# Kernel optimization log

Hardware: AMD Instinct MI355X
Metric: run time of the kernel (lower is better)

The kernel has to match this reference:

```python
import jax, jax.numpy as jnp
import numpy as np

EPS = 1e-5  # torch nn.LayerNorm default

def _ln(x, g, b):
    # LayerNorm over last dim with per-position affine params g, b (broadcastable)
    m = jnp.mean(x, axis=-1, keepdims=True)
    v = jnp.mean((x - m) ** 2, axis=-1, keepdims=True)
    return (x - m) * jax.lax.rsqrt(v + EPS) * g + b

def _mlp_ln(s, W1, b1, W2, b2, g, b):
    # Linear -> SiLU -> Linear -> LayerNorm
    h = jax.nn.silu(s @ W1 + b1) @ W2 + b2
    return _ln(h, g, b)

def setup_inputs() -> dict:
    key = jax.random.key(0)
    B, S, D = 4, 2048, 1024
    MEM, NOI, RES = 512, 64, 32
    ks = jax.random.split(key, 40)
    ki = iter(range(40))
    def nrm(shape, scale=0.02):
        return (jax.random.normal(ks[next(ki)], shape, jnp.float32) * scale)
    def gamma(shape):
        return jnp.ones(shape, jnp.float32) + nrm(shape)
    inp = {
        'x': jax.random.normal(ks[next(ki)], (B, S, D), jnp.float32),
        'pathway_ids': jax.random.randint(ks[next(ki)], (B, S), 0, 1000),
        'compartment_ids': jax.random.randint(ks[next(ki)], (B, S), 0, 5),
        'time_steps': jax.random.randint(ks[next(ki)], (B, S), 0, 5),
        'scale_type': jax.random.randint(ks[next(ki)], (B, S), 0, 3),
        'memory_state': jax.random.normal(ks[next(ki)], (B, MEM), jnp.float32),
        'noise_state': jax.random.normal(ks[next(ki)], (B, NOI), jnp.float32),
        'resource_state': jax.random.normal(ks[next(ki)], (B, RES), jnp.float32),
        # per-pathway / compartment / time / scale LayerNorm affine tables
        'pw_g': gamma((1000, D)), 'pw_b': nrm((1000, D)),
        'cp_g': gamma((5, D)), 'cp_b': nrm((5, D)),
        'tm_g': gamma((5, D)), 'tm_b': nrm((5, D)),
        'ms_g': gamma((3, D)), 'ms_b': nrm((3, D)),
        # memory / stochastic / resource MLP+LN stacks
        'mem_W1': nrm((MEM, D)), 'mem_b1': jnp.zeros((D,)), 'mem_W2': nrm((D, D)), 'mem_b2': jnp.zeros((D,)), 'mem_g': gamma((D,)), 'mem_be': jnp.zeros((D,)),
        'noi_W1': nrm((NOI, D)), 'noi_b1': jnp.zeros((D,)), 'noi_W2': nrm((D, D)), 'noi_b2': jnp.zeros((D,)), 'noi_g': gamma((D,)), 'noi_be': jnp.zeros((D,)),
        'res_W1': nrm((RES, D)), 'res_b1': jnp.zeros((D,)), 'res_W2': nrm((D, D)), 'res_b2': jnp.zeros((D,)), 'res_g': gamma((D,)), 'res_be': jnp.zeros((D,)),
        # integration MLP+LN
        'int_W1': nrm((6 * D, D)), 'int_b1': jnp.zeros((D,)), 'int_W2': nrm((D, D)), 'int_b2': jnp.zeros((D,)), 'int_g': gamma((D,)), 'int_be': jnp.zeros((D,)),
        'aw': jnp.ones((6,), jnp.float32) / 6.0,
    }
    return inp

def reference(x, pathway_ids, compartment_ids, time_steps, scale_type,
              memory_state, noise_state, resource_state,
              pw_g, pw_b, cp_g, cp_b, tm_g, tm_b, ms_g, ms_b,
              mem_W1, mem_b1, mem_W2, mem_b2, mem_g, mem_be,
              noi_W1, noi_b1, noi_W2, noi_b2, noi_g, noi_be,
              res_W1, res_b1, res_W2, res_b2, res_g, res_be,
              int_W1, int_b1, int_W2, int_b2, int_g, int_be, aw):
    # hierarchical: pathway-indexed LN, then compartment-indexed LN on its output
    h = _ln(x, pw_g[pathway_ids], pw_b[pathway_ids])
    h = _ln(h, cp_g[compartment_ids], cp_b[compartment_ids])
    # temporal: time-step-indexed LN of x
    t = _ln(x, tm_g[time_steps], tm_b[time_steps])
    # state-conditioned additive effects, broadcast over seq
    m = x + _mlp_ln(memory_state, mem_W1, mem_b1, mem_W2, mem_b2, mem_g, mem_be)[:, None, :]
    n = x + _mlp_ln(noise_state, noi_W1, noi_b1, noi_W2, noi_b2, noi_g, noi_be)[:, None, :]
    r = x + _mlp_ln(resource_state, res_W1, res_b1, res_W2, res_b2, res_g, res_be)[:, None, :]
    # multiscale: scale-indexed LN (scale in {0,1,2})
    s = _ln(x, ms_g[scale_type], ms_b[scale_type])
    w = jax.nn.softmax(aw)
    cat = jnp.concatenate([w[0] * h, w[1] * t, w[2] * m, w[3] * n, w[4] * r, w[5] * s], axis=-1)
    return _mlp_ln(cat, int_W1, int_b1, int_W2, int_b2, int_g, int_be)
```

## Files before the change

### kernel.cpp

```cpp
#include <hip/hip_runtime.h>
#include <cstdint>
#include <cstddef>

#define EPS_LN 1e-5f

typedef short bf16x8 __attribute__((ext_vector_type(8)));
typedef float f32x4 __attribute__((ext_vector_type(4)));
typedef unsigned int u32_gl __attribute__((address_space(1)));
typedef unsigned int u32_ld __attribute__((address_space(3)));

__device__ __forceinline__ unsigned short f2bf(float f) {
  union { float f; unsigned u; } v; v.f = f;
  unsigned r = v.u + 0x7fffu + ((v.u >> 16) & 1u);
  return (unsigned short)(r >> 16);
}

__device__ __forceinline__ float block_sum256(float v, float* red) {
  for (int m = 32; m > 0; m >>= 1) v += __shfl_xor(v, m, 64);
  const int lane = threadIdx.x & 63, w = threadIdx.x >> 6;
  if (lane == 0) red[w] = v;
  __syncthreads();
  float r = red[0] + red[1] + red[2] + red[3];
  __syncthreads();
  return r;
}

__global__ void prep_w(const float* __restrict__ aw, float* __restrict__ w) {
  if (threadIdx.x == 0) {
    float m = aw[0];
    for (int i = 1; i < 6; ++i) m = fmaxf(m, aw[i]);
    float e[6], s = 0.f;
    for (int i = 0; i < 6; ++i) { e[i] = __expf(aw[i] - m); s += e[i]; }
    for (int i = 0; i < 6; ++i) w[i] = e[i] / s;
  }
}

__global__ __launch_bounds__(256) void init_h1(
    const float* __restrict__ mb1, const float* __restrict__ nb1,
    const float* __restrict__ rb1, float* __restrict__ H1pre) {
  const int idx = blockIdx.x * 256 + threadIdx.x;
  const int row = idx >> 10, j = idx & 1023;
  const int st = row >> 2;
  const float* b1 = st == 0 ? mb1 : st == 1 ? nb1 : rb1;
  H1pre[idx] = b1[j];
}

__global__ __launch_bounds__(256) void state_h1_acc(
    const float* __restrict__ mem, const float* __restrict__ noi, const float* __restrict__ res,
    const float* __restrict__ mW1, const float* __restrict__ nW1, const float* __restrict__ rW1,
    float* __restrict__ H1pre) {
  const int chunk = blockIdx.x, ks = blockIdx.y;
  const int j = chunk * 128 + (threadIdx.x & 127);
  const int half = threadIdx.x >> 7;
  int st, k0, klen, sstride;
  const float* W1; const float* sp;
  if (ks < 8)       { st = 0; W1 = mW1; sp = mem; sstride = 512; k0 = ks * 64 + half * 32; klen = 32; }
  else if (ks == 8) { st = 1; W1 = nW1; sp = noi; sstride = 64;  k0 = half * 32;           klen = 32; }
  else              { st = 2; W1 = rW1; sp = res; sstride = 32;  k0 = half * 16;           klen = 16; }
  float a0 = 0.f, a1 = 0.f, a2 = 0.f, a3 = 0.f;
  const float* wp = W1 + (size_t)k0 * 1024 + j;
  for (int it = 0; it < klen; ++it) {
    const float wv = wp[(size_t)it * 1024];
    const int k = k0 + it;
    a0 += sp[k] * wv;
    a1 += sp[sstride + k] * wv;
    a2 += sp[2 * sstride + k] * wv;
    a3 += sp[3 * sstride + k] * wv;
  }
  __shared__ float part[4][128];
  const int jl = threadIdx.x & 127;
  if (half) { part[0][jl] = a0; part[1][jl] = a1; part[2][jl] = a2; part[3][jl] = a3; }
  __syncthreads();
  if (!half) {
    atomicAdd(&H1pre[(size_t)(st * 4 + 0) * 1024 + j], a0 + part[0][jl]);
    atomicAdd(&H1pre[(size_t)(st * 4 + 1) * 1024 + j], a1 + part[1][jl]);
    atomicAdd(&H1pre[(size_t)(st * 4 + 2) * 1024 + j], a2 + part[2][jl]);
    atomicAdd(&H1pre[(size_t)(st * 4 + 3) * 1024 + j], a3 + part[3][jl]);
  }
}

__global__ __launch_bounds__(256) void h1_silu(
    const float* __restrict__ H1pre, float* __restrict__ H1) {
  const int idx = blockIdx.x * 256 + threadIdx.x;
  const float h = H1pre[idx];
  H1[idx] = h / (1.f + __expf(-h));
}

__global__ __launch_bounds__(256) void init_ys(
    const float* __restrict__ mb2, const float* __restrict__ nb2,
    const float* __restrict__ rb2, float* __restrict__ Ys) {
  const int idx = blockIdx.x * 256 + threadIdx.x;
  const int row = idx >> 10, j = idx & 1023;
  const int st = row >> 2;
  const float* b2 = st == 0 ? mb2 : st == 1 ? nb2 : rb2;
  Ys[idx] = b2[j];
}

__global__ __launch_bounds__(256) void state_y_acc(
    const float* __restrict__ H1,
    const float* __restrict__ mW2, const float* __restrict__ nW2, const float* __restrict__ rW2,
    float* __restrict__ Ys) {
  const int chunk = blockIdx.x, ks = blockIdx.y, st = blockIdx.z;
  const float* W2 = st == 0 ? mW2 : st == 1 ? nW2 : rW2;
  const int j = chunk * 128 + (threadIdx.x & 127);
  const int half = threadIdx.x >> 7;
  const int k0 = ks * 64 + half * 32;
  const float* h1 = H1 + (size_t)st * 4096;
  float a0 = 0.f, a1 = 0.f, a2 = 0.f, a3 = 0.f;
  const float* wp = W2 + (size_t)k0 * 1024 + j;
  for (int it = 0; it < 32; ++it) {
    const float wv = wp[(size_t)it * 1024];
    const int k = k0 + it;
    a0 += h1[k] * wv;
    a1 += h1[1024 + k] * wv;
    a2 += h1[2048 + k] * wv;
    a3 += h1[3072 + k] * wv;
  }
  __shared__ float part[4][128];
  const int jl = threadIdx.x & 127;
  if (half) { part[0][jl] = a0; part[1][jl] = a1; part[2][jl] = a2; part[3][jl] = a3; }
  __syncthreads();
  if (!half) {
    atomicAdd(&Ys[(size_t)(st * 4 + 0) * 1024 + j], a0 + part[0][jl]);
    atomicAdd(&Ys[(size_t)(st * 4 + 1) * 1024 + j], a1 + part[1][jl]);
    atomicAdd(&Ys[(size_t)(st * 4 + 2) * 1024 + j], a2 + part[2][jl]);
    atomicAdd(&Ys[(size_t)(st * 4 + 3) * 1024 + j], a3 + part[3][jl]);
  }
}

__global__ __launch_bounds__(256) void state_ln(
    const float* __restrict__ Ys,
    const float* __restrict__ mg, const float* __restrict__ mbe,
    const float* __restrict__ ng, const float* __restrict__ nbe,
    const float* __restrict__ rg, const float* __restrict__ rbe,
    const float* __restrict__ w, float* __restrict__ mnrv) {
  __shared__ float red[4];
  const int st = blockIdx.x >> 2, b = blockIdx.x & 3;
  const float* g  = st == 0 ? mg  : st == 1 ? ng  : rg;
  const float* be = st == 0 ? mbe : st == 1 ? nbe : rbe;
  const float* y = Ys + (size_t)blockIdx.x * 1024;
  const int j = threadIdx.x * 4;
  float4 yv4 = *(const float4*)(y + j);
  float yv[4] = { yv4.x, yv4.y, yv4.z, yv4.w };
  float s = yv[0] + yv[1] + yv[2] + yv[3];
  float ss = yv[0]*yv[0] + yv[1]*yv[1] + yv[2]*yv[2] + yv[3]*yv[3];
  s = block_sum256(s, red);
  ss = block_sum256(ss, red);
  const float mu = s * (1.f / 1024.f);
  const float rstd = rsqrtf(ss * (1.f / 1024.f) - mu * mu + EPS_LN);
  float4 g4 = *(const float4*)(g + j);
  float4 b4 = *(const float4*)(be + j);
  const float sc = w[2 + st];
  float* out = mnrv + (size_t)b * 3072 + st * 1024;
  out[j]     = ((yv[0] - mu) * rstd * g4.x + b4.x) * sc;
  out[j + 1] = ((yv[1] - mu) * rstd * g4.y + b4.y) * sc;
  out[j + 2] = ((yv[2] - mu) * rstd * g4.z + b4.z) * sc;
  out[j + 3] = ((yv[3] - mu) * rstd * g4.w + b4.w) * sc;
}

__global__ __launch_bounds__(256) void init_bias1(
    const float* __restrict__ ib1, float* __restrict__ bias1) {
  const int j = blockIdx.x * 256 + threadIdx.x;
  bias1[j] = ib1[j & 1023];
}

__global__ __launch_bounds__(256) void bias1_kernel(
    const float* __restrict__ mnrv, const float* __restrict__ iW1,
    float* __restrict__ bias1) {
  const int chunk = blockIdx.x, ks = blockIdx.y;
  const int j = chunk * 128 + (threadIdx.x & 127);
  const int half = threadIdx.x >> 7;
  const int g0 = ks * 64 + half * 32;
  float acc0 = 0.f, acc1 = 0.f, acc2 = 0.f, acc3 = 0.f;
  const float* wp = iW1 + (size_t)(2048 + g0) * 1024 + j;
  for (int it = 0; it < 32; ++it) {
    const int g = g0 + it;
    const float wv = wp[(size_t)it * 1024];
    acc0 += mnrv[g] * wv;
    acc1 += mnrv[3072 + g] * wv;
    acc2 += mnrv[6144 + g] * wv;
    acc3 += mnrv[9216 + g] * wv;
  }
  __shared__ float part[4][128];
  const int jl = threadIdx.x & 127;
  if (half) { part[0][jl] = acc0; part[1][jl] = acc1; part[2][jl] = acc2; part[3][jl] = acc3; }
  __syncthreads();
  if (!half) {
    atomicAdd(&bias1[j],        acc0 + part[0][jl]);
    atomicAdd(&bias1[1024 + j], acc1 + part[1][jl]);
    atomicAdd(&bias1[2048 + j], acc2 + part[2][jl]);
    atomicAdd(&bias1[3072 + j], acc3 + part[3][jl]);
  }
}

__global__ __launch_bounds__(256) void build_w1t(
    const float* __restrict__ W1, const float* __restrict__ w,
    unsigned short* __restrict__ W1T) {
  __shared__ float tile[32][33];
  const int k0 = blockIdx.x * 32, n0 = blockIdx.y * 32;
  const int r = threadIdx.x >> 3;
  const int c = (threadIdx.x & 7) * 4;
  const int kk = k0 + r;
  float v[4];
  if (kk < 2048) {
    const float s = (kk < 1024) ? w[0] : w[1];
    float4 a = *(const float4*)(W1 + (size_t)kk * 1024 + n0 + c);
    v[0] = s * a.x; v[1] = s * a.y; v[2] = s * a.z; v[3] = s * a.w;
  } else if (kk < 3072) {
    const float s2 = w[2], s3 = w[3], s4 = w[4];
    float4 a = *(const float4*)(W1 + (size_t)kk * 1024 + n0 + c);
    float4 bq = *(const float4*)(W1 + (size_t)(kk + 1024) * 1024 + n0 + c);
    float4 cq = *(const float4*)(W1 + (size_t)(kk + 2048) * 1024 + n0 + c);
    v[0] = s2 * a.x + s3 * bq.x + s4 * cq.x;
    v[1] = s2 * a.y + s3 * bq.y + s4 * cq.y;
    v[2] = s2 * a.z + s3 * bq.z + s4 * cq.z;
    v[3] = s2 * a.w + s3 * bq.w + s4 * cq.w;
  } else {
    const float s = w[5];
    float4 a = *(const float4*)(W1 + (size_t)(kk + 2048) * 1024 + n0 + c);
    v[0] = s * a.x; v[1] = s * a.y; v[2] = s * a.z; v[3] = s * a.w;
  }
  tile[r][c] = v[0]; tile[r][c + 1] = v[1]; tile[r][c + 2] = v[2]; tile[r][c + 3] = v[3];
  __syncthreads();
  const int nl = threadIdx.x >> 3;
  const int k4 = (threadIdx.x & 7) * 4;
  ushort4 o;
  o.x = f2bf(tile[k4][nl]);     o.y = f2bf(tile[k4 + 1][nl]);
  o.z = f2bf(tile[k4 + 2][nl]); o.w = f2bf(tile[k4 + 3][nl]);
  *(ushort4*)(W1T + (size_t)(n0 + nl) * 4096 + k0 + k4) = o;
}

__global__ __launch_bounds__(256) void build_w2t(
    const float* __restrict__ W2, unsigned short* __restrict__ W2T) {
  __shared__ float tile[32][33];
  const int k0 = blockIdx.x * 32, n0 = blockIdx.y * 32;
  const int r = threadIdx.x >> 3, c = (threadIdx.x & 7) * 4;
  float4 a = *(const float4*)(W2 + (size_t)(k0 + r) * 1024 + n0 + c);
  tile[r][c] = a.x; tile[r][c + 1] = a.y; tile[r][c + 2] = a.z; tile[r][c + 3] = a.w;
  __syncthreads();
  const int nl = threadIdx.x >> 3, k4 = (threadIdx.x & 7) * 4;
  ushort4 o;
  o.x = f2bf(tile[k4][nl]);     o.y = f2bf(tile[k4 + 1][nl]);
  o.z = f2bf(tile[k4 + 2][nl]); o.w = f2bf(tile[k4 + 3][nl]);
  *(ushort4*)(W2T + (size_t)(n0 + nl) * 1024 + k0 + k4) = o;
}

__global__ __launch_bounds__(256) void build_cat(
    const float* __restrict__ x,
    const int* __restrict__ pid_, const int* __restrict__ cid_,
    const int* __restrict__ tid_, const int* __restrict__ sid_,
    const float* __restrict__ pwg, const float* __restrict__ pwb,
    const float* __restrict__ cpg, const float* __restrict__ cpb,
    const float* __restrict__ tmg, const float* __restrict__ tmb,
    const float* __restrict__ msg, const float* __restrict__ msb,
    unsigned short* __restrict__ cat4) {
  __shared__ float red[4];
  const int row = blockIdx.x;
  const int j = threadIdx.x * 4;
  float4 xv4 = *(const float4*)(x + (size_t)row * 1024 + j);
  float xv[4] = { xv4.x, xv4.y, xv4.z, xv4.w };
  float s = xv[0] + xv[1] + xv[2] + xv[3];
  float ss = xv[0]*xv[0] + xv[1]*xv[1] + xv[2]*xv[2] + xv[3]*xv[3];
  s = block_sum256(s, red);
  ss = block_sum256(ss, red);
  const float mu = s * (1.f / 1024.f);
  const float rstd = rsqrtf(ss * (1.f / 1024.f) - mu * mu + EPS_LN);
  float xh[4];
  for (int q = 0; q < 4; ++q) xh[q] = (xv[q] - mu) * rstd;
  const int pid = pid_[row], cid = cid_[row], tmi = tid_[row], msi = sid_[row];
  unsigned short* crow = cat4 + (size_t)row * 4096;

  float4 g4 = *(const float4*)(pwg + (size_t)pid * 1024 + j);
  float4 b4 = *(const float4*)(pwb + (size_t)pid * 1024 + j);
  float h1[4];
  h1[0] = xh[0] * g4.x + b4.x; h1[1] = xh[1] * g4.y + b4.y;
  h1[2] = xh[2] * g4.z + b4.z; h1[3] = xh[3] * g4.w + b4.w;
  float s1 = h1[0] + h1[1] + h1[2] + h1[3];
  float ss1 = h1[0]*h1[0] + h1[1]*h1[1] + h1[2]*h1[2] + h1[3]*h1[3];
  s1 = block_sum256(s1, red);
  ss1 = block_sum256(ss1, red);
  const float mu1 = s1 * (1.f / 1024.f);
  const float rstd1 = rsqrtf(ss1 * (1.f / 1024.f) - mu1 * mu1 + EPS_LN);
  g4 = *(const float4*)(cpg + (size_t)cid * 1024 + j);
  b4 = *(const float4*)(cpb + (size_t)cid * 1024 + j);
  ushort4 o;
  o.x = f2bf((h1[0] - mu1) * rstd1 * g4.x + b4.x);
  o.y = f2bf((h1[1] - mu1) * rstd1 * g4.y + b4.y);
  o.z = f2bf((h1[2] - mu1) * rstd1 * g4.z + b4.z);
  o.w = f2bf((h1[3] - mu1) * rstd1 * g4.w + b4.w);
  *(ushort4*)(crow + j) = o;

  g4 = *(const float4*)(tmg + (size_t)tmi * 1024 + j);
  b4 = *(const float4*)(tmb + (size_t)tmi * 1024 + j);
  o.x = f2bf(xh[0] * g4.x + b4.x); o.y = f2bf(xh[1] * g4.y + b4.y);
  o.z = f2bf(xh[2] * g4.z + b4.z); o.w = f2bf(xh[3] * g4.w + b4.w);
  *(ushort4*)(crow + 1024 + j) = o;

  o.x = f2bf(xv[0]); o.y = f2bf(xv[1]); o.z = f2bf(xv[2]); o.w = f2bf(xv[3]);
  *(ushort4*)(crow + 2048 + j) = o;

  g4 = *(const float4*)(msg + (size_t)msi * 1024 + j);
  b4 = *(const float4*)(msb + (size_t)msi * 1024 + j);
  o.x = f2bf(xh[0] * g4.x + b4.x); o.y = f2bf(xh[1] * g4.y + b4.y);
  o.z = f2bf(xh[2] * g4.z + b4.z); o.w = f2bf(xh[3] * g4.w + b4.w);
  *(ushort4*)(crow + 3072 + j) = o;
}

template <int EPI>
__global__ __launch_bounds__(256, 2) void gemm_bt(
    const unsigned short* __restrict__ A, const unsigned short* __restrict__ BT,
    const float* __restrict__ bias, void* __restrict__ out, int K) {
  __shared__ unsigned short At[128 * 32];
  __shared__ unsigned short Bt[128 * 32];
  const int t = threadIdx.x;
  const int lane = t & 63;
  const int wave = t >> 6;
  const int wr = wave >> 1, wc = wave & 1;
  const int quad = lane >> 4, l16 = lane & 15;
  const int bm = blockIdx.x, bn = blockIdx.y;
  const unsigned short* Ab = A + (size_t)bm * 128 * K;
  const unsigned short* Bb = BT + (size_t)bn * 128 * K;
  const int r0 = t >> 2, c0 = (t & 3) * 8;
  f32x4 acc[4][4];
#pragma unroll
  for (int i = 0; i < 4; ++i)
#pragma unroll
    for (int jj = 0; jj < 4; ++jj) { f32x4 z = {0.f, 0.f, 0.f, 0.f}; acc[i][jj] = z; }

  for (int kt = 0; kt < K; kt += 32) {
    __builtin_amdgcn_global_load_lds(
        (const u32_gl*)(Ab + (size_t)r0 * K + kt + c0),
        (u32_ld*)(At + t * 8), 16, 0, 0);
    __builtin_amdgcn_global_load_lds(
        (const u32_gl*)(Ab + (size_t)(r0 + 64) * K + kt + c0),
        (u32_ld*)(At + (256 + t) * 8), 16, 0, 0);
    __builtin_amdgcn_global_load_lds(
        (const u32_gl*)(Bb + (size_t)r0 * K + kt + c0),
        (u32_ld*)(Bt + t * 8), 16, 0, 0);
    __builtin_amdgcn_global_load_lds(
        (const u32_gl*)(Bb + (size_t)(r0 + 64) * K + kt + c0),
        (u32_ld*)(Bt + (256 + t) * 8), 16, 0, 0);
    __syncthreads();
    bf16x8 aF[4], bF[4];
#pragma unroll
    for (int mi = 0; mi < 4; ++mi)
      aF[mi] = *(const bf16x8*)(At + (wr * 64 + mi * 16 + l16) * 32 + quad * 8);
#pragma unroll
    for (int ni = 0; ni < 4; ++ni)
      bF[ni] = *(const bf16x8*)(Bt + (wc * 64 + ni * 16 + l16) * 32 + quad * 8);
#pragma unroll
    for (int mi = 0; mi < 4; ++mi)
#pragma unroll
      for (int ni = 0; ni < 4; ++ni)
        acc[mi][ni] = __builtin_amdgcn_mfma_f32_16x16x32_bf16(aF[mi], bF[ni], acc[mi][ni], 0, 0, 0);
    __syncthreads();
  }
#pragma unroll
  for (int mi = 0; mi < 4; ++mi) {
#pragma unroll
    for (int ni = 0; ni < 4; ++ni) {
      const int col = bn * 128 + wc * 64 + ni * 16 + l16;
#pragma unroll
      for (int r = 0; r < 4; ++r) {
        const int row = bm * 128 + wr * 64 + mi * 16 + quad * 4 + r;
        float v = acc[mi][ni][r];
        if (EPI == 1) {
          v += bias[(size_t)(row >> 11) * 1024 + col];
          v = v / (1.f + __expf(-v));
          ((unsigned short*)out)[(size_t)row * 1024 + col] = f2bf(v);
        } else {
          v += bias[col];
          ((float*)out)[(size_t)row * 1024 + col] = v;
        }
      }
    }
  }
}

__global__ __launch_bounds__(256) void final_ln(
    const float* __restrict__ Y, const float* __restrict__ g,
    const float* __restrict__ be, float* __restrict__ out) {
  __shared__ float red[4];
  const int row = blockIdx.x;
  const int j = threadIdx.x * 4;
  float4 yv4 = *(const float4*)(Y + (size_t)row * 1024 + j);
  float yv[4] = { yv4.x, yv4.y, yv4.z, yv4.w };
  float s = yv[0] + yv[1] + yv[2] + yv[3];
  float ss = yv[0]*yv[0] + yv[1]*yv[1] + yv[2]*yv[2] + yv[3]*yv[3];
  s = block_sum256(s, red);
  ss = block_sum256(ss, red);
  const float mu = s * (1.f / 1024.f);
  const float rstd = rsqrtf(ss * (1.f / 1024.f) - mu * mu + EPS_LN);
  float4 g4 = *(const float4*)(g + j);
  float4 b4 = *(const float4*)(be + j);
  float4 o;
  o.x = (yv[0] - mu) * rstd * g4.x + b4.x;
  o.y = (yv[1] - mu) * rstd * g4.y + b4.y;
  o.z = (yv[2] - mu) * rstd * g4.z + b4.z;
  o.w = (yv[3] - mu) * rstd * g4.w + b4.w;
  *(float4*)(out + (size_t)row * 1024 + j) = o;
}

extern "C" void kernel_launch(void* const* d_in, const int* in_sizes, int n_in,
                              void* d_out, int out_size, void* d_ws, size_t ws_size,
                              hipStream_t stream) {
  const float* x   = (const float*)d_in[0];
  const int*   pid = (const int*)d_in[1];
  const int*   cid = (const int*)d_in[2];
  const int*   tms = (const int*)d_in[3];
  const int*   sct = (const int*)d_in[4];
  const float* mem = (const float*)d_in[5];
  const float* noi = (const float*)d_in[6];
  const float* res = (const float*)d_in[7];
  const float* pwg = (const float*)d_in[8];
  const float* pwb = (const float*)d_in[9];
  const float* cpg = (const float*)d_in[10];
  const float* cpb = (const float*)d_in[11];
  const float* tmg = (const float*)d_in[12];
  const float* tmb = (const float*)d_in[13];
  const float* msg = (const float*)d_in[14];
  const float* msb = (const float*)d_in[15];
  const float* mW1 = (const float*)d_in[16]; const float* mb1 = (const float*)d_in[17];
  const float* mW2 = (const float*)d_in[18]; const float* mb2 = (const float*)d_in[19];
  const float* mg  = (const float*)d_in[20]; const float* mbe = (const float*)d_in[21];
  const float* nW1 = (const float*)d_in[22]; const float* nb1 = (const float*)d_in[23];
  const float* nW2 = (const float*)d_in[24]; const float* nb2 = (const float*)d_in[25];
  const float* ng  = (const float*)d_in[26]; const float* nbe = (const float*)d_in[27];
  const float* rW1 = (const float*)d_in[28]; const float* rb1 = (const float*)d_in[29];
  const float* rW2 = (const float*)d_in[30]; const float* rb2 = (const float*)d_in[31];
  const float* rg  = (const float*)d_in[32]; const float* rbe = (const float*)d_in[33];
  const float* iW1 = (const float*)d_in[34]; const float* ib1 = (const float*)d_in[35];
  const float* iW2 = (const float*)d_in[36]; const float* ib2 = (const float*)d_in[37];
  const float* ig  = (const float*)d_in[38]; const float* ibe = (const float*)d_in[39];
  const float* aw  = (const float*)d_in[40];

  char* ws = (char*)d_ws;
  float* w6    = (float*)ws;
  float* H1pre = w6 + 16;
  float* H1    = H1pre + 12288;
  float* Ys    = H1 + 12288;
  float* mnrv  = Ys + 12288;
  float* bias1 = mnrv + 12288;
  unsigned short* W1T  = (unsigned short*)(ws + (1ull << 20));
  unsigned short* W2T  = (unsigned short*)(ws + (9ull << 20));
  unsigned short* cat4 = (unsigned short*)(ws + (11ull << 20));
  unsigned short* Hb   = (unsigned short*)(ws + (75ull << 20));
  float* Ybuf          = (float*)cat4;

  prep_w<<<1, 64, 0, stream>>>(aw, w6);
  init_h1<<<48, 256, 0, stream>>>(mb1, nb1, rb1, H1pre);
  state_h1_acc<<<dim3(8, 10), 256, 0, stream>>>(mem, noi, res, mW1, nW1, rW1, H1pre);
  h1_silu<<<48, 256, 0, stream>>>(H1pre, H1);
  init_ys<<<48, 256, 0, stream>>>(mb2, nb2, rb2, Ys);
  state_y_acc<<<dim3(8, 16, 3), 256, 0, stream>>>(H1, mW2, nW2, rW2, Ys);
  state_ln<<<12, 256, 0, stream>>>(Ys, mg, mbe, ng, nbe, rg, rbe, w6, mnrv);
  init_bias1<<<16, 256, 0, stream>>>(ib1, bias1);
  bias1_kernel<<<dim3(8, 48), 256, 0, stream>>>(mnrv, iW1, bias1);
  build_w1t<<<dim3(128, 32), 256, 0, stream>>>(iW1, w6, W1T);
  build_w2t<<<dim3(32, 32), 256, 0, stream>>>(iW2, W2T);
  build_cat<<<8192, 256, 0, stream>>>(x, pid, cid, tms, sct,
                                      pwg, pwb, cpg, cpb, tmg, tmb, msg, msb, cat4);
  gemm_bt<1><<<dim3(64, 8), 256, 0, stream>>>(cat4, W1T, bias1, (void*)Hb, 4096);
  gemm_bt<2><<<dim3(64, 8), 256, 0, stream>>>(Hb, W2T, ib2, (void*)Ybuf, 1024);
  final_ln<<<8192, 256, 0, stream>>>(Ybuf, ig, ibe, (float*)d_out);
}
```

Before: 384.8 us.

## Merge small setup kernels, fuse SiLU into state GEMV, shrink GEMM tile

Four tiny initialization kernels (softmax weights and three bias broadcasts) are merged into one launch, and the SiLU pass is folded into the second state GEMV so H1 is no longer stored and reloaded. The main bf16 MFMA GEMMs switch from 128x128 tiles with 4 waves to 64x128 tiles with 2 waves and 128 threads. This doubles the block count to 1024 per GEMM for better CU coverage, at the cost of lower A/B reuse per tile and more global loads per thread. SiLU is now recomputed in every ks/chunk block of the state GEMV.

```diff
diff --git a/kernel.cpp b/kernel.cpp
--- a/kernel.cpp
+++ b/kernel.cpp
@@ -25,24 +25,40 @@
   return r;
 }
 
-__global__ void prep_w(const float* __restrict__ aw, float* __restrict__ w) {
-  if (threadIdx.x == 0) {
-    float m = aw[0];
-    for (int i = 1; i < 6; ++i) m = fmaxf(m, aw[i]);
-    float e[6], s = 0.f;
-    for (int i = 0; i < 6; ++i) { e[i] = __expf(aw[i] - m); s += e[i]; }
-    for (int i = 0; i < 6; ++i) w[i] = e[i] / s;
-  }
-}
-
-__global__ __launch_bounds__(256) void init_h1(
-    const float* __restrict__ mb1, const float* __restrict__ nb1,
-    const float* __restrict__ rb1, float* __restrict__ H1pre) {
-  const int idx = blockIdx.x * 256 + threadIdx.x;
-  const int row = idx >> 10, j = idx & 1023;
-  const int st = row >> 2;
-  const float* b1 = st == 0 ? mb1 : st == 1 ? nb1 : rb1;
-  H1pre[idx] = b1[j];
+__global__ __launch_bounds__(256) void setup_small(
+    const float* __restrict__ aw,
+    const float* __restrict__ mb1, const float* __restrict__ nb1, const float* __restrict__ rb1,
+    const float* __restrict__ mb2, const float* __restrict__ nb2, const float* __restrict__ rb2,
+    const float* __restrict__ ib1,
+    float* __restrict__ w, float* __restrict__ H1pre, float* __restrict__ Ys,
+    float* __restrict__ bias1) {
+  const int bi = blockIdx.x;
+  if (bi == 0) {
+    if (threadIdx.x == 0) {
+      float m = aw[0];
+      for (int i = 1; i < 6; ++i) m = fmaxf(m, aw[i]);
+      float e[6], s = 0.f;
+      for (int i = 0; i < 6; ++i) { e[i] = __expf(aw[i] - m); s += e[i]; }
+      for (int i = 0; i < 6; ++i) w[i] = e[i] / s;
+    }
+    return;
+  }
+  if (bi <= 48) {
+    const int idx = (bi - 1) * 256 + threadIdx.x;
+    const int st = idx >> 12;
+    const float* b1 = st == 0 ? mb1 : st == 1 ? nb1 : rb1;
+    H1pre[idx] = b1[idx & 1023];
+    return;
+  }
+  if (bi <= 96) {
+    const int idx = (bi - 49) * 256 + threadIdx.x;
+    const int st = idx >> 12;
+    const float* b2 = st == 0 ? mb2 : st == 1 ? nb2 : rb2;
+    Ys[idx] = b2[idx & 1023];
+    return;
+  }
+  const int idx = (bi - 97) * 256 + threadIdx.x;
+  bias1[idx] = ib1[idx & 1023];
 }
 
 __global__ __launch_bounds__(256) void state_h1_acc(
@@ -79,25 +95,8 @@
   }
 }
 
-__global__ __launch_bounds__(256) void h1_silu(
-    const float* __restrict__ H1pre, float* __restrict__ H1) {
-  const int idx = blockIdx.x * 256 + threadIdx.x;
-  const float h = H1pre[idx];
-  H1[idx] = h / (1.f + __expf(-h));
-}
-
-__global__ __launch_bounds__(256) void init_ys(
-    const float* __restrict__ mb2, const float* __restrict__ nb2,
-    const float* __restrict__ rb2, float* __restrict__ Ys) {
-  const int idx = blockIdx.x * 256 + threadIdx.x;
-  const int row = idx >> 10, j = idx & 1023;
-  const int st = row >> 2;
-  const float* b2 = st == 0 ? mb2 : st == 1 ? nb2 : rb2;
-  Ys[idx] = b2[j];
-}
-
 __global__ __launch_bounds__(256) void state_y_acc(
-    const float* __restrict__ H1,
+    const float* __restrict__ H1pre,
     const float* __restrict__ mW2, const float* __restrict__ nW2, const float* __restrict__ rW2,
     float* __restrict__ Ys) {
   const int chunk = blockIdx.x, ks = blockIdx.y, st = blockIdx.z;
@@ -105,16 +104,17 @@
   const int j = chunk * 128 + (threadIdx.x & 127);
   const int half = threadIdx.x >> 7;
   const int k0 = ks * 64 + half * 32;
-  const float* h1 = H1 + (size_t)st * 4096;
+  const float* h1 = H1pre + (size_t)st * 4096;
   float a0 = 0.f, a1 = 0.f, a2 = 0.f, a3 = 0.f;
   const float* wp = W2 + (size_t)k0 * 1024 + j;
   for (int it = 0; it < 32; ++it) {
     const float wv = wp[(size_t)it * 1024];
     const int k = k0 + it;
-    a0 += h1[k] * wv;
-    a1 += h1[1024 + k] * wv;
-    a2 += h1[2048 + k] * wv;
-    a3 += h1[3072 + k] * wv;
+    float h;
+    h = h1[k];        a0 += (h / (1.f + __expf(-h))) * wv;
+    h = h1[1024 + k]; a1 += (h / (1.f + __expf(-h))) * wv;
+    h = h1[2048 + k]; a2 += (h / (1.f + __expf(-h))) * wv;
+    h = h1[3072 + k]; a3 += (h / (1.f + __expf(-h))) * wv;
   }
   __shared__ float part[4][128];
   const int jl = threadIdx.x & 127;
@@ -158,12 +158,6 @@
   out[j + 3] = ((yv[3] - mu) * rstd * g4.w + b4.w) * sc;
 }
 
-__global__ __launch_bounds__(256) void init_bias1(
-    const float* __restrict__ ib1, float* __restrict__ bias1) {
-  const int j = blockIdx.x * 256 + threadIdx.x;
-  bias1[j] = ib1[j & 1023];
-}
-
 __global__ __launch_bounds__(256) void bias1_kernel(
     const float* __restrict__ mnrv, const float* __restrict__ iW1,
     float* __restrict__ bias1) {
@@ -307,18 +301,17 @@
 }
 
 template <int EPI>
-__global__ __launch_bounds__(256, 2) void gemm_bt(
+__global__ __launch_bounds__(128, 4) void gemm_bt(
     const unsigned short* __restrict__ A, const unsigned short* __restrict__ BT,
     const float* __restrict__ bias, void* __restrict__ out, int K) {
-  __shared__ unsigned short At[128 * 32];
+  __shared__ unsigned short At[64 * 32];
   __shared__ unsigned short Bt[128 * 32];
   const int t = threadIdx.x;
   const int lane = t & 63;
-  const int wave = t >> 6;
-  const int wr = wave >> 1, wc = wave & 1;
+  const int wc = t >> 6;
   const int quad = lane >> 4, l16 = lane & 15;
   const int bm = blockIdx.x, bn = blockIdx.y;
-  const unsigned short* Ab = A + (size_t)bm * 128 * K;
+  const unsigned short* Ab = A + (size_t)bm * 64 * K;
   const unsigned short* Bb = BT + (size_t)bn * 128 * K;
   const int r0 = t >> 2, c0 = (t & 3) * 8;
   f32x4 acc[4][4];
@@ -332,19 +325,25 @@
         (const u32_gl*)(Ab + (size_t)r0 * K + kt + c0),
         (u32_ld*)(At + t * 8), 16, 0, 0);
     __builtin_amdgcn_global_load_lds(
-        (const u32_gl*)(Ab + (size_t)(r0 + 64) * K + kt + c0),
-        (u32_ld*)(At + (256 + t) * 8), 16, 0, 0);
+        (const u32_gl*)(Ab + (size_t)(r0 + 32) * K + kt + c0),
+        (u32_ld*)(At + (128 + t) * 8), 16, 0, 0);
     __builtin_amdgcn_global_load_lds(
         (const u32_gl*)(Bb + (size_t)r0 * K + kt + c0),
         (u32_ld*)(Bt + t * 8), 16, 0, 0);
     __builtin_amdgcn_global_load_lds(
+        (const u32_gl*)(Bb + (size_t)(r0 + 32) * K + kt + c0),
+        (u32_ld*)(Bt + (128 + t) * 8), 16, 0, 0);
+    __builtin_amdgcn_global_load_lds(
         (const u32_gl*)(Bb + (size_t)(r0 + 64) * K + kt + c0),
         (u32_ld*)(Bt + (256 + t) * 8), 16, 0, 0);
+    __builtin_amdgcn_global_load_lds(
+        (const u32_gl*)(Bb + (size_t)(r0 + 96) * K + kt + c0),
+        (u32_ld*)(Bt + (384 + t) * 8), 16, 0, 0);
     __syncthreads();
     bf16x8 aF[4], bF[4];
 #pragma unroll
     for (int mi = 0; mi < 4; ++mi)
-      aF[mi] = *(const bf16x8*)(At + (wr * 64 + mi * 16 + l16) * 32 + quad * 8);
+      aF[mi] = *(const bf16x8*)(At + (mi * 16 + l16) * 32 + quad * 8);
 #pragma unroll
     for (int ni = 0; ni < 4; ++ni)
       bF[ni] = *(const bf16x8*)(Bt + (wc * 64 + ni * 16 + l16) * 32 + quad * 8);
@@ -362,7 +361,7 @@
       const int col = bn * 128 + wc * 64 + ni * 16 + l16;
 #pragma unroll
       for (int r = 0; r < 4; ++r) {
-        const int row = bm * 128 + wr * 64 + mi * 16 + quad * 4 + r;
+        const int row = bm * 64 + mi * 16 + quad * 4 + r;
         float v = acc[mi][ni][r];
         if (EPI == 1) {
           v += bias[(size_t)(row >> 11) * 1024 + col];
@@ -437,8 +436,7 @@
   char* ws = (char*)d_ws;
   float* w6    = (float*)ws;
   float* H1pre = w6 + 16;
-  float* H1    = H1pre + 12288;
-  float* Ys    = H1 + 12288;
+  float* Ys    = H1pre + 12288;
   float* mnrv  = Ys + 12288;
   float* bias1 = mnrv + 12288;
   unsigned short* W1T  = (unsigned short*)(ws + (1ull << 20));
@@ -447,20 +445,17 @@
   unsigned short* Hb   = (unsigned short*)(ws + (75ull << 20));
   float* Ybuf          = (float*)cat4;
 
-  prep_w<<<1, 64, 0, stream>>>(aw, w6);
-  init_h1<<<48, 256, 0, stream>>>(mb1, nb1, rb1, H1pre);
+  setup_small<<<113, 256, 0, stream>>>(aw, mb1, nb1, rb1, mb2, nb2, rb2, ib1,
+                                       w6, H1pre, Ys, bias1);
   state_h1_acc<<<dim3(8, 10), 256, 0, stream>>>(mem, noi, res, mW1, nW1, rW1, H1pre);
-  h1_silu<<<48, 256, 0, stream>>>(H1pre, H1);
-  init_ys<<<48, 256, 0, stream>>>(mb2, nb2, rb2, Ys);
-  state_y_acc<<<dim3(8, 16, 3), 256, 0, stream>>>(H1, mW2, nW2, rW2, Ys);
+  state_y_acc<<<dim3(8, 16, 3), 256, 0, stream>>>(H1pre, mW2, nW2, rW2, Ys);
   state_ln<<<12, 256, 0, stream>>>(Ys, mg, mbe, ng, nbe, rg, rbe, w6, mnrv);
-  init_bias1<<<16, 256, 0, stream>>>(ib1, bias1);
   bias1_kernel<<<dim3(8, 48), 256, 0, stream>>>(mnrv, iW1, bias1);
   build_w1t<<<dim3(128, 32), 256, 0, stream>>>(iW1, w6, W1T);
   build_w2t<<<dim3(32, 32), 256, 0, stream>>>(iW2, W2T);
   build_cat<<<8192, 256, 0, stream>>>(x, pid, cid, tms, sct,
                                       pwg, pwb, cpg, cpb, tmg, tmb, msg, msb, cat4);
-  gemm_bt<1><<<dim3(64, 8), 256, 0, stream>>>(cat4, W1T, bias1, (void*)Hb, 4096);
-  gemm_bt<2><<<dim3(64, 8), 256, 0, stream>>>(Hb, W2T, ib2, (void*)Ybuf, 1024);
+  gemm_bt<1><<<dim3(128, 8), 128, 0, stream>>>(cat4, W1T, bias1, (void*)Hb, 4096);
+  gemm_bt<2><<<dim3(128, 8), 128, 0, stream>>>(Hb, W2T, ib2, (void*)Ybuf, 1024);
   final_ln<<<8192, 256, 0, stream>>>(Ybuf, ig, ibe, (float*)d_out);
 }
```

Measured after the change: 405.6 us. 5.4% more time.
